# Kernel tuning notes

Measured on AMD Instinct MI355X. Metric: run time of the kernel, lower is better.

## Reference

```python
import jax, jax.numpy as jnp
import numpy as np


def setup_inputs() -> dict:
    key = jax.random.key(0)
    B, D = 4096, 1024
    ks = jax.random.split(key, 4)
    return {
        "text_embed": jax.random.normal(ks[0], (B, D), dtype=jnp.float32),
        "image_embed": jax.random.normal(ks[1], (B, D), dtype=jnp.float32),
        "audio_embed": jax.random.normal(ks[2], (B, D), dtype=jnp.float32),
        "depth_embed": jax.random.normal(ks[3], (B, D), dtype=jnp.float32),
        # CLIP-style temperature already exponentiated (~100 at convergence)
        "logit_scale": jnp.ones((1,), dtype=jnp.float32) * 100.0,
    }


def _contrastive_pair(feat1, feat2_all, logit_scale):
    # logits[i,j] = scale * <feat1_i, feat2_j>; labels = arange(B) -> diagonal
    logits = logit_scale * (feat1 @ feat2_all.T)          # [B, B]
    logp = jax.nn.log_softmax(logits, axis=-1)
    return -jnp.mean(jnp.diagonal(logp))


def reference(text_embed, image_embed, audio_embed, depth_embed, logit_scale):
    s = logit_scale[0]
    total = jnp.float32(0.0)
    for m_emb in (audio_embed, depth_embed):
        # modality <-> text
        l_m2t = _contrastive_pair(m_emb, text_embed, s)
        l_t2m = _contrastive_pair(text_embed, m_emb, s)
        total = total + (l_m2t + l_t2m) / 2
        # modality <-> image
        l_m2i = _contrastive_pair(m_emb, image_embed, s)
        l_i2m = _contrastive_pair(image_embed, m_emb, s)
        total = total + (l_m2i + l_i2m) / 2
    # text <-> image
    l_t2i = _contrastive_pair(text_embed, image_embed, s)
    l_i2t = _contrastive_pair(image_embed, text_embed, s)
    total = total + (l_t2i + l_i2t) / 2
    return total
```

## Files before the change

### kernel.cpp

```cpp
#include <hip/hip_runtime.h>
#include <hip/hip_bf16.h>

#define BDIM 4096
#define DDIM 1024
#define NPAIRS 5
#define TW 16
#define KT 16
#define RSH 8192

typedef __attribute__((ext_vector_type(8))) short short8;
typedef __attribute__((ext_vector_type(4))) float floatx4;

__device__ __forceinline__ void gload16(const void* g, void* l) {
    __builtin_amdgcn_global_load_lds((const __attribute__((address_space(1))) void*)g,
                                     (__attribute__((address_space(3))) void*)l, 16, 0, 0);
}

__device__ __forceinline__ unsigned short f2bf(float f) {
    unsigned u = __float_as_uint(f);
    u = (u + 0x7FFFu + ((u >> 16) & 1u)) >> 16;
    return (unsigned short)u;
}

__global__ void cast_kernel(const float* __restrict__ t, const float* __restrict__ im,
                            const float* __restrict__ au, const float* __restrict__ de,
                            short* __restrict__ out) {
    const float* src;
    switch (blockIdx.y) {
        case 0: src = t; break;
        case 1: src = im; break;
        case 2: src = au; break;
        default: src = de; break;
    }
    short* dst = out + (size_t)blockIdx.y * (BDIM * DDIM);
    int idx = (blockIdx.x * 256 + threadIdx.x) * 8;
    float4 f0 = *(const float4*)(src + idx);
    float4 f1 = *(const float4*)(src + idx + 4);
    short8 r;
    r[0] = (short)f2bf(f0.x); r[1] = (short)f2bf(f0.y);
    r[2] = (short)f2bf(f0.z); r[3] = (short)f2bf(f0.w);
    r[4] = (short)f2bf(f1.x); r[5] = (short)f2bf(f1.y);
    r[6] = (short)f2bf(f1.z); r[7] = (short)f2bf(f1.w);
    *(short8*)(dst + idx) = r;
}

__device__ __forceinline__ void stage_region(const short* __restrict__ gsrc, short* reg,
                                             int w, int l, int k0) {
    const int r0 = w * 16 + (l >> 2);
    const int kof = ((l & 3) ^ ((l >> 3) & 3)) * 8;
#pragma unroll
    for (int i = 0; i < 2; ++i) {
        gload16(gsrc + (size_t)(i * 128 + r0) * DDIM + k0 + kof,
                (char*)reg + i * 8192 + w * 1024 + l * 16);
    }
}

__device__ __forceinline__ short8 ldsfrag32(const short* reg, int row, int hi) {
    return *(const short8*)((const char*)reg + row * 64 + ((hi ^ ((row >> 1) & 3)) << 4));
}

__device__ __forceinline__ float vsel4(floatx4 v, int j) {
    return (j == 0) ? v[0] : (j == 1) ? v[1] : (j == 2) ? v[2] : v[3];
}

#define SBAR()  do { __builtin_amdgcn_sched_barrier(0); __builtin_amdgcn_s_barrier(); } while (0)
#define WAITVL(vm) do { asm volatile("s_waitcnt vmcnt(" #vm ") lgkmcnt(0)" ::: "memory"); \
                        __builtin_amdgcn_sched_barrier(0); } while (0)
#define WAITL() do { asm volatile("s_waitcnt lgkmcnt(0)" ::: "memory"); \
                     __builtin_amdgcn_sched_barrier(0); } while (0)

#define MFMA8x2(NB) do { __builtin_amdgcn_s_setprio(1); \
    _Pragma("unroll") for (int m_ = 0; m_ < 8; ++m_) { \
        acc[m_][NB]     = __builtin_amdgcn_mfma_f32_16x16x32_bf16(afr[m_], b0, acc[m_][NB], 0, 0, 0); \
        acc[m_][NB + 1] = __builtin_amdgcn_mfma_f32_16x16x32_bf16(afr[m_], b1, acc[m_][NB + 1], 0, 0, 0); } \
    __builtin_amdgcn_s_setprio(0); } while (0)

#define TILE_BODY(T, VM0, VM2, S0, S1, S2, S3) do { \
    const short* Ar0 = As + (((T) & 1) * 2 + 0) * RSH; \
    const short* Br0 = Bs + (((T) & 1) * 2 + 0) * RSH; \
    const short* Ar1 = As + (((T) & 1) * 2 + 1) * RSH; \
    const short* Br1 = Bs + (((T) & 1) * 2 + 1) * RSH; \
     \
    _Pragma("unroll") for (int m_ = 0; m_ < 8; ++m_) afr[m_] = ldsfrag32(Ar0, arow + m_ * 16, hi); \
    b0 = ldsfrag32(Br0, brow + 0, hi); b1 = ldsfrag32(Br0, brow + 16, hi); \
    if (S0) stage_region(Bop, Bs + ((((T) + 1) & 1) * 2 + 1) * RSH, w, l, ((T) + 1) * 64 + 32); \
    SBAR(); WAITVL(VM0); MFMA8x2(0); SBAR(); \
     \
    b0 = ldsfrag32(Br0, brow + 32, hi); b1 = ldsfrag32(Br0, brow + 48, hi); \
    if (S1) stage_region(Aop, As + (((T) & 1) * 2 + 0) * RSH, w, l, ((T) + 2) * 64); \
    SBAR(); WAITL(); MFMA8x2(2); SBAR(); \
     \
    _Pragma("unroll") for (int m_ = 0; m_ < 8; ++m_) afr[m_] = ldsfrag32(Ar1, arow + m_ * 16, hi); \
    b0 = ldsfrag32(Br1, brow + 0, hi); b1 = ldsfrag32(Br1, brow + 16, hi); \
    if (S2) stage_region(Bop, Bs + (((T) & 1) * 2 + 0) * RSH, w, l, ((T) + 2) * 64); \
    SBAR(); WAITVL(VM2); MFMA8x2(0); SBAR(); \
     \
    b0 = ldsfrag32(Br1, brow + 32, hi); b1 = ldsfrag32(Br1, brow + 48, hi); \
    if (S3) stage_region(Aop, As + (((T) & 1) * 2 + 1) * RSH, w, l, ((T) + 2) * 64 + 32); \
    SBAR(); WAITL(); MFMA8x2(2); SBAR(); \
} while (0)

__launch_bounds__(512, 1)
__global__ void gemm_lse_kernel(const short* __restrict__ mats, const float* __restrict__ scale_p,
                                float* __restrict__ rowpart, float* __restrict__ colpart,
                                float* __restrict__ diag) {
    extern __shared__ char smem[];
    short* As = (short*)smem;
    short* Bs = (short*)(smem + 65536);
    float* rowLse = (float*)(smem + 131072);
    float* colLse = rowLse + 4 * 256;

    const int tid = threadIdx.x;
    const int w = tid >> 6, l = tid & 63;
    const int wr = w >> 2, wc = w & 3;

    const int orig = blockIdx.x;
    const int swz = (orig & 7) * 160 + (orig >> 3);
    const int p = swz >> 8;
    const int t = swz & 255;
    const int tileRow = t & 15, tileCol = t >> 4;

    int ai, bi;
    switch (p) {
        case 0: ai = 2; bi = 0; break;
        case 1: ai = 2; bi = 1; break;
        case 2: ai = 3; bi = 0; break;
        case 3: ai = 3; bi = 1; break;
        default: ai = 0; bi = 1; break;
    }
    const short* Aop = mats + (size_t)ai * (BDIM * DDIM) + tileRow * 256 * DDIM;
    const short* Bop = mats + (size_t)bi * (BDIM * DDIM) + tileCol * 256 * DDIM;

    floatx4 acc[8][4];
#pragma unroll
    for (int m = 0; m < 8; ++m)
#pragma unroll
        for (int n = 0; n < 4; ++n) acc[m][n] = (floatx4)(0.f);

    const int fr = l & 15, hi = l >> 4;
    const int arow = wr * 128 + fr;
    const int brow = wc * 64 + fr;

    short8 afr[8], b0, b1;

    stage_region(Aop, As + 0 * RSH, w, l, 0);
    stage_region(Bop, Bs + 0 * RSH, w, l, 0);
    stage_region(Aop, As + 1 * RSH, w, l, 32);
    stage_region(Bop, Bs + 1 * RSH, w, l, 32);
    stage_region(Aop, As + 2 * RSH, w, l, 64);
    stage_region(Bop, Bs + 2 * RSH, w, l, 64);
    stage_region(Aop, As + 3 * RSH, w, l, 96);
    asm volatile("s_waitcnt vmcnt(10)" ::: "memory");
    __builtin_amdgcn_s_barrier();

#pragma unroll 2
    for (int kt = 0; kt < 14; ++kt) TILE_BODY(kt, 8, 8, 1, 1, 1, 1);
    TILE_BODY(14, 8, 4, 1, 0, 0, 0);
    TILE_BODY(15, 0, 0, 0, 0, 0, 0);

    const float s = scale_p[0];
#pragma unroll
    for (int m = 0; m < 8; ++m)
#pragma unroll
        for (int n = 0; n < 4; ++n)
#pragma unroll
            for (int j = 0; j < 4; ++j) acc[m][n][j] *= s;


#pragma unroll
    for (int m = 0; m < 8; ++m) {
#pragma unroll
        for (int j = 0; j < 4; ++j) {
            float mx = -3.0e38f;
#pragma unroll
            for (int n = 0; n < 4; ++n) mx = fmaxf(mx, acc[m][n][j]);
#pragma unroll
            for (int off = 1; off < 16; off <<= 1) mx = fmaxf(mx, __shfl_xor(mx, off));
            float sm = 0.f;
#pragma unroll
            for (int n = 0; n < 4; ++n) sm += __expf(acc[m][n][j] - mx);
#pragma unroll
            for (int off = 1; off < 16; off <<= 1) sm += __shfl_xor(sm, off);
            if (fr == 0)
                rowLse[wc * 256 + wr * 128 + m * 16 + hi * 4 + j] = mx + __logf(sm);
        }
    }

#pragma unroll
    for (int n = 0; n < 4; ++n) {
        float mx = -3.0e38f;
#pragma unroll
        for (int m = 0; m < 8; ++m)
#pragma unroll
            for (int j = 0; j < 4; ++j) mx = fmaxf(mx, acc[m][n][j]);
        mx = fmaxf(mx, __shfl_xor(mx, 16));
        mx = fmaxf(mx, __shfl_xor(mx, 32));
        float sm = 0.f;
#pragma unroll
        for (int m = 0; m < 8; ++m)
#pragma unroll
            for (int j = 0; j < 4; ++j) sm += __expf(acc[m][n][j] - mx);
        sm += __shfl_xor(sm, 16);
        sm += __shfl_xor(sm, 32);
        if (hi == 0)
            colLse[wr * 256 + wc * 64 + n * 16 + fr] = mx + __logf(sm);
    }

    if (tileRow == tileCol && (wc >> 1) == wr) {
        if (hi == (fr >> 2)) {
            const int j = fr & 3;
            float* dst = diag + p * BDIM + tileRow * 256 + wc * 64 + fr;
            if ((wc & 1) == 0) {
                dst[0]  = vsel4(acc[0][0], j);
                dst[16] = vsel4(acc[1][1], j);
                dst[32] = vsel4(acc[2][2], j);
                dst[48] = vsel4(acc[3][3], j);
            } else {
                dst[0]  = vsel4(acc[4][0], j);
                dst[16] = vsel4(acc[5][1], j);
                dst[32] = vsel4(acc[6][2], j);
                dst[48] = vsel4(acc[7][3], j);
            }
        }
    }

    __syncthreads();

    if (tid < 256) {
        float v0 = rowLse[tid], v1 = rowLse[256 + tid], v2 = rowLse[512 + tid], v3 = rowLse[768 + tid];
        float mm = fmaxf(fmaxf(v0, v1), fmaxf(v2, v3));
        float r = mm + __logf(__expf(v0 - mm) + __expf(v1 - mm) + __expf(v2 - mm) + __expf(v3 - mm));
        rowpart[((size_t)p * BDIM + tileRow * 256 + tid) * TW + tileCol] = r;
    } else {
        int c = tid - 256;
        float v0 = colLse[c], v1 = colLse[256 + c];
        float mm = fmaxf(v0, v1);
        float r = mm + __logf(__expf(v0 - mm) + __expf(v1 - mm));
        colpart[((size_t)p * BDIM + tileCol * 256 + c) * TW + tileRow] = r;
    }
}

__global__ void reduce_kernel(const float* __restrict__ rowpart, const float* __restrict__ colpart,
                              const float* __restrict__ diag, float* __restrict__ partials) {
    int p = blockIdx.y;
    int i = blockIdx.x * 256 + threadIdx.x;
    size_t gi = (size_t)p * BDIM + i;

    const float* rp = rowpart + gi * TW;
    float mx = -3.0e38f;
#pragma unroll
    for (int t = 0; t < TW; ++t) mx = fmaxf(mx, rp[t]);
    float sm = 0.f;
#pragma unroll
    for (int t = 0; t < TW; ++t) sm += __expf(rp[t] - mx);
    float rl = mx + __logf(sm);

    const float* cp = colpart + gi * TW;
    mx = -3.0e38f;
#pragma unroll
    for (int t = 0; t < TW; ++t) mx = fmaxf(mx, cp[t]);
    sm = 0.f;
#pragma unroll
    for (int t = 0; t < TW; ++t) sm += __expf(cp[t] - mx);
    float cl = mx + __logf(sm);

    float contrib = rl + cl - 2.f * diag[gi];

    __shared__ float red[256];
    red[threadIdx.x] = contrib;
    __syncthreads();
    for (int s2 = 128; s2 > 0; s2 >>= 1) {
        if (threadIdx.x < (unsigned)s2) red[threadIdx.x] += red[threadIdx.x + s2];
        __syncthreads();
    }
    if (threadIdx.x == 0) partials[p * 16 + blockIdx.x] = red[0];
}

__global__ void final_kernel(const float* __restrict__ partials, float* __restrict__ out) {
    __shared__ float red[128];
    int t = threadIdx.x;
    red[t] = (t < NPAIRS * 16) ? partials[t] : 0.f;
    __syncthreads();
    for (int s2 = 64; s2 > 0; s2 >>= 1) {
        if (t < s2) red[t] += red[t + s2];
        __syncthreads();
    }
    if (t == 0) out[0] = red[0] * (1.f / (2.f * BDIM));
}

extern "C" void kernel_launch(void* const* d_in, const int* in_sizes, int n_in,
                              void* d_out, int out_size, void* d_ws, size_t ws_size,
                              hipStream_t stream) {
    const float* text  = (const float*)d_in[0];
    const float* image = (const float*)d_in[1];
    const float* audio = (const float*)d_in[2];
    const float* depth = (const float*)d_in[3];
    const float* scale = (const float*)d_in[4];
    float* out = (float*)d_out;

    char* ws = (char*)d_ws;
    short* mats = (short*)ws;
    size_t off = (size_t)4 * BDIM * DDIM * 2;
    float* rowpart = (float*)(ws + off); off += (size_t)NPAIRS * BDIM * TW * 4;
    float* colpart = (float*)(ws + off); off += (size_t)NPAIRS * BDIM * TW * 4;
    float* diag    = (float*)(ws + off); off += (size_t)NPAIRS * BDIM * 4;
    float* partials= (float*)(ws + off); off += NPAIRS * 16 * 4;

    const int smem_bytes = 131072 + 4 * 256 * 4 + 2 * 256 * 4;
    hipFuncSetAttribute((const void*)gemm_lse_kernel,
                        hipFuncAttributeMaxDynamicSharedMemorySize, smem_bytes);

    cast_kernel<<<dim3(2048, 4), 256, 0, stream>>>(text, image, audio, depth, mats);
    gemm_lse_kernel<<<dim3(1280), 512, smem_bytes, stream>>>(mats, scale, rowpart, colpart, diag);
    reduce_kernel<<<dim3(16, NPAIRS), 256, 0, stream>>>(rowpart, colpart, diag, partials);
    final_kernel<<<1, 128, 0, stream>>>(partials, out);
}
```

Baseline: 234.2 us.

## Prefetch LDS fragments one phase ahead with double-buffered registers in GEMM loop

Restructures the MFMA main loop so each phase's LDS fragment loads (A and B) are issued one phase ahead into double-buffered register sets (afr0/afr1, bA/bB). The MFMAs then only wait for older LDS reads via partial lgkmcnt counts, and the vmcnt waits are split from the LDS waits. The aim is to hide LDS read latency behind MFMA execution. The cost is more VGPR pressure from doubled fragment registers, and the hand-tuned wait counts must match the exact number of outstanding loads to stay correct.

```diff
diff --git a/kernel.cpp b/kernel.cpp
--- a/kernel.cpp
+++ b/kernel.cpp
@@ -64,40 +64,52 @@
 }
 
 #define SBAR()  do { __builtin_amdgcn_sched_barrier(0); __builtin_amdgcn_s_barrier(); } while (0)
-#define WAITVL(vm) do { asm volatile("s_waitcnt vmcnt(" #vm ") lgkmcnt(0)" ::: "memory"); \
-                        __builtin_amdgcn_sched_barrier(0); } while (0)
-#define WAITL() do { asm volatile("s_waitcnt lgkmcnt(0)" ::: "memory"); \
-                     __builtin_amdgcn_sched_barrier(0); } while (0)
-
-#define MFMA8x2(NB) do { __builtin_amdgcn_s_setprio(1); \
+#define WAITV_(n) do { asm volatile("s_waitcnt vmcnt(" #n ")" ::: "memory"); \
+                       __builtin_amdgcn_sched_barrier(0); } while (0)
+#define WAITV(n) WAITV_(n)
+#define WAITL_(n) do { asm volatile("s_waitcnt lgkmcnt(" #n ")" ::: "memory"); \
+                       __builtin_amdgcn_sched_barrier(0); } while (0)
+#define WAITL(n) WAITL_(n)
+
+#define MFMA_PH(AFR, BV0, BV1, NB) do { __builtin_amdgcn_s_setprio(1); \
     _Pragma("unroll") for (int m_ = 0; m_ < 8; ++m_) { \
-        acc[m_][NB]     = __builtin_amdgcn_mfma_f32_16x16x32_bf16(afr[m_], b0, acc[m_][NB], 0, 0, 0); \
-        acc[m_][NB + 1] = __builtin_amdgcn_mfma_f32_16x16x32_bf16(afr[m_], b1, acc[m_][NB + 1], 0, 0, 0); } \
+        acc[m_][NB]     = __builtin_amdgcn_mfma_f32_16x16x32_bf16(AFR[m_], BV0, acc[m_][NB], 0, 0, 0); \
+        acc[m_][NB + 1] = __builtin_amdgcn_mfma_f32_16x16x32_bf16(AFR[m_], BV1, acc[m_][NB + 1], 0, 0, 0); } \
     __builtin_amdgcn_s_setprio(0); } while (0)
 
-#define TILE_BODY(T, VM0, VM2, S0, S1, S2, S3) do { \
-    const short* Ar0 = As + (((T) & 1) * 2 + 0) * RSH; \
-    const short* Br0 = Bs + (((T) & 1) * 2 + 0) * RSH; \
-    const short* Ar1 = As + (((T) & 1) * 2 + 1) * RSH; \
-    const short* Br1 = Bs + (((T) & 1) * 2 + 1) * RSH; \
+#define TILE_BODY(T, W0, VM0, W2, VM2, S0, S1, S2, S3, R3) do { \
+    const short* Ab  = As + (((T) & 1) * 2) * RSH; \
+    const short* Bb  = Bs + (((T) & 1) * 2) * RSH; \
+    const short* AbN = As + ((((T) + 1) & 1) * 2) * RSH; \
+    const short* BbN = Bs + ((((T) + 1) & 1) * 2) * RSH; \
      \
-    _Pragma("unroll") for (int m_ = 0; m_ < 8; ++m_) afr[m_] = ldsfrag32(Ar0, arow + m_ * 16, hi); \
-    b0 = ldsfrag32(Br0, brow + 0, hi); b1 = ldsfrag32(Br0, brow + 16, hi); \
+    bB0 = ldsfrag32(Bb, brow + 32, hi); \
+    bB1 = ldsfrag32(Bb, brow + 48, hi); \
     if (S0) stage_region(Bop, Bs + ((((T) + 1) & 1) * 2 + 1) * RSH, w, l, ((T) + 1) * 64 + 32); \
-    SBAR(); WAITVL(VM0); MFMA8x2(0); SBAR(); \
+    if (W0) WAITV(VM0); \
+    SBAR(); WAITL(2); MFMA_PH(afr0, bA0, bA1, 0); SBAR(); \
      \
-    b0 = ldsfrag32(Br0, brow + 32, hi); b1 = ldsfrag32(Br0, brow + 48, hi); \
+    _Pragma("unroll") for (int m_ = 0; m_ < 8; ++m_) afr1[m_] = ldsfrag32(Ab + RSH, arow + m_ * 16, hi); \
+    bA0 = ldsfrag32(Bb + RSH, brow + 0, hi); \
+    bA1 = ldsfrag32(Bb + RSH, brow + 16, hi); \
     if (S1) stage_region(Aop, As + (((T) & 1) * 2 + 0) * RSH, w, l, ((T) + 2) * 64); \
-    SBAR(); WAITL(); MFMA8x2(2); SBAR(); \
+    SBAR(); WAITL(10); MFMA_PH(afr0, bB0, bB1, 2); SBAR(); \
      \
-    _Pragma("unroll") for (int m_ = 0; m_ < 8; ++m_) afr[m_] = ldsfrag32(Ar1, arow + m_ * 16, hi); \
-    b0 = ldsfrag32(Br1, brow + 0, hi); b1 = ldsfrag32(Br1, brow + 16, hi); \
+    bB0 = ldsfrag32(Bb + RSH, brow + 32, hi); \
+    bB1 = ldsfrag32(Bb + RSH, brow + 48, hi); \
     if (S2) stage_region(Bop, Bs + (((T) & 1) * 2 + 0) * RSH, w, l, ((T) + 2) * 64); \
-    SBAR(); WAITVL(VM2); MFMA8x2(0); SBAR(); \
+    if (W2) WAITV(VM2); \
+    SBAR(); WAITL(2); MFMA_PH(afr1, bA0, bA1, 0); SBAR(); \
      \
-    b0 = ldsfrag32(Br1, brow + 32, hi); b1 = ldsfrag32(Br1, brow + 48, hi); \
+    if (R3) { \
+        _Pragma("unroll") for (int m_ = 0; m_ < 8; ++m_) afr0[m_] = ldsfrag32(AbN, arow + m_ * 16, hi); \
+        bA0 = ldsfrag32(BbN, brow + 0, hi); \
+        bA1 = ldsfrag32(BbN, brow + 16, hi); \
+    } \
     if (S3) stage_region(Aop, As + (((T) & 1) * 2 + 1) * RSH, w, l, ((T) + 2) * 64 + 32); \
-    SBAR(); WAITL(); MFMA8x2(2); SBAR(); \
+    SBAR(); \
+    if (R3) { WAITL(10); } else { WAITL(0); } \
+    MFMA_PH(afr1, bB0, bB1, 2); SBAR(); \
 } while (0)
 
 __launch_bounds__(512, 1)
@@ -141,7 +153,7 @@
     const int arow = wr * 128 + fr;
     const int brow = wc * 64 + fr;
 
-    short8 afr[8], b0, b1;
+    short8 afr0[8], afr1[8], bA0, bA1, bB0, bB1;
 
     stage_region(Aop, As + 0 * RSH, w, l, 0);
     stage_region(Bop, Bs + 0 * RSH, w, l, 0);
@@ -150,13 +162,19 @@
     stage_region(Aop, As + 2 * RSH, w, l, 64);
     stage_region(Bop, Bs + 2 * RSH, w, l, 64);
     stage_region(Aop, As + 3 * RSH, w, l, 96);
-    asm volatile("s_waitcnt vmcnt(10)" ::: "memory");
-    __builtin_amdgcn_s_barrier();
+    WAITV(10);
+    SBAR();
+    {
+#pragma unroll
+        for (int m_ = 0; m_ < 8; ++m_) afr0[m_] = ldsfrag32(As, arow + m_ * 16, hi);
+        bA0 = ldsfrag32(Bs, brow + 0, hi);
+        bA1 = ldsfrag32(Bs, brow + 16, hi);
+    }
 
 #pragma unroll 2
-    for (int kt = 0; kt < 14; ++kt) TILE_BODY(kt, 8, 8, 1, 1, 1, 1);
-    TILE_BODY(14, 8, 4, 1, 0, 0, 0);
-    TILE_BODY(15, 0, 0, 0, 0, 0, 0);
+    for (int kt = 0; kt < 14; ++kt) TILE_BODY(kt, 1, 8, 1, 8, 1, 1, 1, 1, 1);
+    TILE_BODY(14, 1, 8, 1, 4, 1, 0, 0, 0, 1);
+    TILE_BODY(15, 1, 0, 0, 0, 0, 0, 0, 0, 0);
 
     const float s = scale_p[0];
 #pragma unroll
```

After: 241.8 us. 1.03x slower.
